# Kernel optimization log

Measured on AMD Instinct MI355X. Metric: run time of the kernel, lower is better.

## Reference

```python
import jax, jax.numpy as jnp
import numpy as np

BATCH, TIME, IN, HID = 32, 512, 512, 1024
THRESHOLD = 1.0
BETA = 1.0 / 2.0  # 1/tau


def setup_inputs() -> dict:
    key = jax.random.key(0)
    kx, kw, kb = jax.random.split(key, 3)
    x = jax.random.normal(kx, (BATCH, TIME, IN), dtype=jnp.float32)
    bound = 1.0 / np.sqrt(IN)  # nn.Linear default init range
    W = jax.random.uniform(kw, (HID, IN), minval=-bound, maxval=bound, dtype=jnp.float32)
    b = jax.random.uniform(kb, (HID,), minval=-bound, maxval=bound, dtype=jnp.float32)
    return {"x": x, "W": W, "b": b}


def reference(x, W, b):
    # Precompute all per-step linear projections in one big GEMM: [B,T,H]
    hidden = jnp.einsum("bti,hi->bth", x, W) + b

    def step(mem, h_t):
        # h_t: [B,H]
        mem = BETA * mem + h_t
        spk = (mem > THRESHOLD).astype(h_t.dtype)
        mem = mem * (1.0 - spk)  # hard reset
        return mem, spk

    mem0 = jnp.zeros((x.shape[0], W.shape[0]), dtype=x.dtype)
    # scan over time: [T,B,H]
    _, spikes = jax.lax.scan(step, mem0, jnp.swapaxes(hidden, 0, 1))
    return jnp.swapaxes(spikes, 0, 1)  # [B,T,H]
```

## Files before the change

kernel.cpp:

```cpp
#include <hip/hip_runtime.h>

#define BATCH 32
#define TIME  512
#define INF   512
#define HIDF  1024

#define MBT  128
#define NBH  128
#define KCH  16
#define NCH  (INF / KCH)
#define TILEF (MBT * KCH)

#define GLD16(g, l) __builtin_amdgcn_global_load_lds(                      \
    (const __attribute__((address_space(1))) void*)(g),                    \
    (__attribute__((address_space(3))) void*)(l), 16, 0, 0)

__global__ __launch_bounds__(256, 2)
void snn_gemm_seqfma(const float* __restrict__ x, const float* __restrict__ W,
                     const float* __restrict__ bias, float* __restrict__ hidden) {
    __shared__ __align__(16) float xs[2 * TILEF];
    __shared__ __align__(16) float ws[2 * TILEF];

    const int tid = threadIdx.x;
    const int l   = tid & 63;
    const int wv  = __builtin_amdgcn_readfirstlane(tid >> 6);
    const int lx  = l & 7;
    const int ly  = (l >> 3) & 7;
    const int bt0 = blockIdx.y * MBT;
    const int h0  = blockIdx.x * NBH;
    const int wbt = 64 * (wv >> 1);
    const int wh  = 64 * (wv & 1);

    const int rl = l >> 2;
    const int qs = l & 3;
    const int g0 = ((rl & 1) << 3) | (rl >> 1);
    const int wA = 2 * wv;
    const int wB = 2 * wv + 1;
    const int rA = wA * 16 + g0;
    const int rB = wB * 16 + g0;
    const int qA = qs ^ (wA & 3);
    const int qB = qs ^ (wB & 3);
    const float* xgA = x + (size_t)(bt0 + rA) * INF + qA * 4;
    const float* xgB = x + (size_t)(bt0 + rB) * INF + qB * 4;
    const float* wgA = W + (size_t)(h0 + rA) * INF + qA * 4;
    const float* wgB = W + (size_t)(h0 + rB) * INF + qB * 4;
    const int dOffA = (32 * wv) * KCH;
    const int dOffB = dOffA + 16 * KCH;

    GLD16(xgA, xs + dOffA);
    GLD16(xgB, xs + dOffB);
    GLD16(wgA, ws + dOffA);
    GLD16(wgB, ws + dOffB);

    float acc[8][8];
    #pragma unroll
    for (int r = 0; r < 8; ++r)
        #pragma unroll
        for (int c = 0; c < 8; ++c) acc[r][c] = 0.0f;

    __syncthreads();

    const int xrow0 = wbt + (ly >> 1) * 16 + (ly & 1);
    const int wrow0 = wh  + (lx >> 1) * 16 + (lx & 1);
    const int xq = (ly >> 1) & 3;
    const int wq = (lx >> 1) & 3;

    for (int kc = 0; kc < NCH; ++kc) {
        const int p  = kc & 1;
        const int np = p ^ 1;

        if (kc + 1 < NCH) {
            const int so = (kc + 1) * KCH;
            float* xd = xs + np * TILEF;
            float* wd = ws + np * TILEF;
            GLD16(xgA + so, xd + dOffA);
            GLD16(xgB + so, xd + dOffB);
            GLD16(wgA + so, wd + dOffA);
            GLD16(wgB + so, wd + dOffB);
        }

        const float* xb = xs + p * TILEF;
        const float* wb = ws + p * TILEF;
        #pragma unroll
        for (int g = 0; g < 4; ++g) {
            const int gx_ = (g ^ xq) * 4;
            const int gw_ = (g ^ wq) * 4;
            const float* xr = xb + xrow0 * KCH + gx_;
            const float* wr = wb + wrow0 * KCH + gw_;
            float4 xf[8], wf[8];
            #pragma unroll
            for (int r = 0; r < 8; ++r)
                xf[r] = *(const float4*)(xr + r * 2 * KCH);
            #pragma unroll
            for (int c = 0; c < 8; ++c)
                wf[c] = *(const float4*)(wr + c * 2 * KCH);
            #pragma unroll
            for (int r = 0; r < 8; ++r)
                #pragma unroll
                for (int c = 0; c < 8; ++c)
                    acc[r][c] = __fmaf_rn(xf[r].x, wf[c].x, acc[r][c]);
            #pragma unroll
            for (int r = 0; r < 8; ++r)
                #pragma unroll
                for (int c = 0; c < 8; ++c)
                    acc[r][c] = __fmaf_rn(xf[r].y, wf[c].y, acc[r][c]);
            #pragma unroll
            for (int r = 0; r < 8; ++r)
                #pragma unroll
                for (int c = 0; c < 8; ++c)
                    acc[r][c] = __fmaf_rn(xf[r].z, wf[c].z, acc[r][c]);
            #pragma unroll
            for (int r = 0; r < 8; ++r)
                #pragma unroll
                for (int c = 0; c < 8; ++c)
                    acc[r][c] = __fmaf_rn(xf[r].w, wf[c].w, acc[r][c]);
        }
        __syncthreads();
    }

    float bv[8];
    #pragma unroll
    for (int c = 0; c < 8; ++c) bv[c] = bias[h0 + wh + lx * 8 + c];
    #pragma unroll
    for (int r = 0; r < 8; ++r) {
        float* orow = hidden + (size_t)(bt0 + wbt + ly * 8 + r) * HIDF
                             + h0 + wh + lx * 8;
        float4 o0, o1;
        o0.x = __fadd_rn(acc[r][0], bv[0]);
        o0.y = __fadd_rn(acc[r][1], bv[1]);
        o0.z = __fadd_rn(acc[r][2], bv[2]);
        o0.w = __fadd_rn(acc[r][3], bv[3]);
        o1.x = __fadd_rn(acc[r][4], bv[4]);
        o1.y = __fadd_rn(acc[r][5], bv[5]);
        o1.z = __fadd_rn(acc[r][6], bv[6]);
        o1.w = __fadd_rn(acc[r][7], bv[7]);
        ((float4*)orow)[0] = o0;
        ((float4*)orow)[1] = o1;
    }
}

#define SEG 32

__global__ __launch_bounds__(64)
void snn_scan_np(float* __restrict__ io) {
    const int n = blockIdx.x * 64 + threadIdx.x;
    const int b = n >> 10;
    const int h = n & 1023;
    float* p = io + (size_t)b * TIME * HIDF + h;

    float A[SEG], B[SEG];
    float mem = 0.0f;

    #pragma unroll
    for (int u = 0; u < SEG; ++u) A[u] = p[u * HIDF];

    for (int tb = 0; tb < TIME / SEG; tb += 2) {
        #pragma unroll
        for (int u = 0; u < SEG; ++u) B[u] = p[((tb + 1) * SEG + u) * HIDF];
        #pragma unroll
        for (int u = 0; u < SEG; ++u) {
            mem = __fadd_rn(__fmul_rn(0.5f, mem), A[u]);
            const bool s = mem > 1.0f;
            p[(tb * SEG + u) * HIDF] = s ? 1.0f : 0.0f;
            if (s) mem = 0.0f;
        }
        if (tb + 2 < TIME / SEG) {
            #pragma unroll
            for (int u = 0; u < SEG; ++u) A[u] = p[((tb + 2) * SEG + u) * HIDF];
        }
        #pragma unroll
        for (int u = 0; u < SEG; ++u) {
            mem = __fadd_rn(__fmul_rn(0.5f, mem), B[u]);
            const bool s = mem > 1.0f;
            p[((tb + 1) * SEG + u) * HIDF] = s ? 1.0f : 0.0f;
            if (s) mem = 0.0f;
        }
    }
}

extern "C" void kernel_launch(void* const* d_in, const int* in_sizes, int n_in,
                              void* d_out, int out_size, void* d_ws, size_t ws_size,
                              hipStream_t stream) {
    const float* x    = (const float*)d_in[0];
    const float* W    = (const float*)d_in[1];
    const float* bias = (const float*)d_in[2];
    float* out = (float*)d_out;

    dim3 g1(HIDF / NBH, (BATCH * TIME) / MBT);
    snn_gemm_seqfma<<<g1, 256, 0, stream>>>(x, W, bias, out);

    snn_scan_np<<<(BATCH * HIDF) / 64, 64, 0, stream>>>(out);
}
```

Measured before the change: 314.4 us.

## Give each wave private LDS tiles and replace block barriers with vmcnt waits

Each wave now stages its own 64-row slices of x and W into a private double-buffered LDS region. The per-chunk __syncthreads is replaced by a per-wave s_waitcnt vmcnt plus a scheduling barrier, and the last chunk is peeled out of the loop. The aim is to remove block-wide barrier stalls and let waves run independently. In exchange, LDS use per block doubles to 64KB, and x/W rows shared by waves in the same block are now fetched redundantly, which raises global and L2 load traffic.

```diff
diff --git a/kernel.cpp b/kernel.cpp
--- a/kernel.cpp
+++ b/kernel.cpp
@@ -9,17 +9,57 @@
 #define NBH  128
 #define KCH  16
 #define NCH  (INF / KCH)
-#define TILEF (MBT * KCH)
 
 #define GLD16(g, l) __builtin_amdgcn_global_load_lds(                      \
     (const __attribute__((address_space(1))) void*)(g),                    \
     (__attribute__((address_space(3))) void*)(l), 16, 0, 0)
 
+
+__device__ __forceinline__ void compute_chunk(const float* __restrict__ xb,
+                                              const float* __restrict__ wb,
+                                              int xrow0, int wrow0,
+                                              int xq, int wq,
+                                              float acc[8][8]) {
+    #pragma unroll
+    for (int g = 0; g < 4; ++g) {
+        const int gx_ = (g ^ xq) * 4;
+        const int gw_ = (g ^ wq) * 4;
+        const float* xr = xb + xrow0 * KCH + gx_;
+        const float* wr = wb + wrow0 * KCH + gw_;
+        float4 xf[8], wf[8];
+        #pragma unroll
+        for (int r = 0; r < 8; ++r)
+            xf[r] = *(const float4*)(xr + r * 2 * KCH);
+        #pragma unroll
+        for (int c = 0; c < 8; ++c)
+            wf[c] = *(const float4*)(wr + c * 2 * KCH);
+        #pragma unroll
+        for (int r = 0; r < 8; ++r)
+            #pragma unroll
+            for (int c = 0; c < 8; ++c)
+                acc[r][c] = __fmaf_rn(xf[r].x, wf[c].x, acc[r][c]);
+        #pragma unroll
+        for (int r = 0; r < 8; ++r)
+            #pragma unroll
+            for (int c = 0; c < 8; ++c)
+                acc[r][c] = __fmaf_rn(xf[r].y, wf[c].y, acc[r][c]);
+        #pragma unroll
+        for (int r = 0; r < 8; ++r)
+            #pragma unroll
+            for (int c = 0; c < 8; ++c)
+                acc[r][c] = __fmaf_rn(xf[r].z, wf[c].z, acc[r][c]);
+        #pragma unroll
+        for (int r = 0; r < 8; ++r)
+            #pragma unroll
+            for (int c = 0; c < 8; ++c)
+                acc[r][c] = __fmaf_rn(xf[r].w, wf[c].w, acc[r][c]);
+    }
+}
+
 __global__ __launch_bounds__(256, 2)
 void snn_gemm_seqfma(const float* __restrict__ x, const float* __restrict__ W,
                      const float* __restrict__ bias, float* __restrict__ hidden) {
-    __shared__ __align__(16) float xs[2 * TILEF];
-    __shared__ __align__(16) float ws[2 * TILEF];
+    __shared__ __align__(16) float lds[2][4][2][1024];
 
     const int tid = threadIdx.x;
     const int l   = tid & 63;
@@ -34,23 +74,23 @@
     const int rl = l >> 2;
     const int qs = l & 3;
     const int g0 = ((rl & 1) << 3) | (rl >> 1);
-    const int wA = 2 * wv;
-    const int wB = 2 * wv + 1;
-    const int rA = wA * 16 + g0;
-    const int rB = wB * 16 + g0;
-    const int qA = qs ^ (wA & 3);
-    const int qB = qs ^ (wB & 3);
-    const float* xgA = x + (size_t)(bt0 + rA) * INF + qA * 4;
-    const float* xgB = x + (size_t)(bt0 + rB) * INF + qB * 4;
-    const float* wgA = W + (size_t)(h0 + rA) * INF + qA * 4;
-    const float* wgB = W + (size_t)(h0 + rB) * INF + qB * 4;
-    const int dOffA = (32 * wv) * KCH;
-    const int dOffB = dOffA + 16 * KCH;
-
-    GLD16(xgA, xs + dOffA);
-    GLD16(xgB, xs + dOffB);
-    GLD16(wgA, ws + dOffA);
-    GLD16(wgB, ws + dOffB);
+    const float* px0 = x + (size_t)(bt0 + wbt +  0 + g0) * INF + ((qs ^ 0) * 4);
+    const float* px1 = x + (size_t)(bt0 + wbt + 16 + g0) * INF + ((qs ^ 1) * 4);
+    const float* px2 = x + (size_t)(bt0 + wbt + 32 + g0) * INF + ((qs ^ 2) * 4);
+    const float* px3 = x + (size_t)(bt0 + wbt + 48 + g0) * INF + ((qs ^ 3) * 4);
+    const float* pw0 = W + (size_t)(h0 + wh +  0 + g0) * INF + ((qs ^ 0) * 4);
+    const float* pw1 = W + (size_t)(h0 + wh + 16 + g0) * INF + ((qs ^ 1) * 4);
+    const float* pw2 = W + (size_t)(h0 + wh + 32 + g0) * INF + ((qs ^ 2) * 4);
+    const float* pw3 = W + (size_t)(h0 + wh + 48 + g0) * INF + ((qs ^ 3) * 4);
+
+    GLD16(px0, &lds[0][wv][0][0 * 256]);
+    GLD16(px1, &lds[0][wv][0][1 * 256]);
+    GLD16(px2, &lds[0][wv][0][2 * 256]);
+    GLD16(px3, &lds[0][wv][0][3 * 256]);
+    GLD16(pw0, &lds[0][wv][1][0 * 256]);
+    GLD16(pw1, &lds[0][wv][1][1 * 256]);
+    GLD16(pw2, &lds[0][wv][1][2 * 256]);
+    GLD16(pw3, &lds[0][wv][1][3 * 256]);
 
     float acc[8][8];
     #pragma unroll
@@ -58,65 +98,36 @@
         #pragma unroll
         for (int c = 0; c < 8; ++c) acc[r][c] = 0.0f;
 
-    __syncthreads();
-
-    const int xrow0 = wbt + (ly >> 1) * 16 + (ly & 1);
-    const int wrow0 = wh  + (lx >> 1) * 16 + (lx & 1);
+    const int xrow0 = (ly >> 1) * 16 + (ly & 1);
+    const int wrow0 = (lx >> 1) * 16 + (lx & 1);
     const int xq = (ly >> 1) & 3;
     const int wq = (lx >> 1) & 3;
 
-    for (int kc = 0; kc < NCH; ++kc) {
+    for (int kc = 0; kc < NCH - 1; ++kc) {
         const int p  = kc & 1;
         const int np = p ^ 1;
-
-        if (kc + 1 < NCH) {
-            const int so = (kc + 1) * KCH;
-            float* xd = xs + np * TILEF;
-            float* wd = ws + np * TILEF;
-            GLD16(xgA + so, xd + dOffA);
-            GLD16(xgB + so, xd + dOffB);
-            GLD16(wgA + so, wd + dOffA);
-            GLD16(wgB + so, wd + dOffB);
-        }
-
-        const float* xb = xs + p * TILEF;
-        const float* wb = ws + p * TILEF;
-        #pragma unroll
-        for (int g = 0; g < 4; ++g) {
-            const int gx_ = (g ^ xq) * 4;
-            const int gw_ = (g ^ wq) * 4;
-            const float* xr = xb + xrow0 * KCH + gx_;
-            const float* wr = wb + wrow0 * KCH + gw_;
-            float4 xf[8], wf[8];
-            #pragma unroll
-            for (int r = 0; r < 8; ++r)
-                xf[r] = *(const float4*)(xr + r * 2 * KCH);
-            #pragma unroll
-            for (int c = 0; c < 8; ++c)
-                wf[c] = *(const float4*)(wr + c * 2 * KCH);
-            #pragma unroll
-            for (int r = 0; r < 8; ++r)
-                #pragma unroll
-                for (int c = 0; c < 8; ++c)
-                    acc[r][c] = __fmaf_rn(xf[r].x, wf[c].x, acc[r][c]);
-            #pragma unroll
-            for (int r = 0; r < 8; ++r)
-                #pragma unroll
-                for (int c = 0; c < 8; ++c)
-                    acc[r][c] = __fmaf_rn(xf[r].y, wf[c].y, acc[r][c]);
-            #pragma unroll
-            for (int r = 0; r < 8; ++r)
-                #pragma unroll
-                for (int c = 0; c < 8; ++c)
-                    acc[r][c] = __fmaf_rn(xf[r].z, wf[c].z, acc[r][c]);
-            #pragma unroll
-            for (int r = 0; r < 8; ++r)
-                #pragma unroll
-                for (int c = 0; c < 8; ++c)
-                    acc[r][c] = __fmaf_rn(xf[r].w, wf[c].w, acc[r][c]);
-        }
-        __syncthreads();
-    }
+        const int so = (kc + 1) * KCH;
+
+        GLD16(px0 + so, &lds[np][wv][0][0 * 256]);
+        GLD16(px1 + so, &lds[np][wv][0][1 * 256]);
+        GLD16(px2 + so, &lds[np][wv][0][2 * 256]);
+        GLD16(px3 + so, &lds[np][wv][0][3 * 256]);
+        GLD16(pw0 + so, &lds[np][wv][1][0 * 256]);
+        GLD16(pw1 + so, &lds[np][wv][1][1 * 256]);
+        GLD16(pw2 + so, &lds[np][wv][1][2 * 256]);
+        GLD16(pw3 + so, &lds[np][wv][1][3 * 256]);
+
+        asm volatile("s_waitcnt vmcnt(8)" ::: "memory");
+        __builtin_amdgcn_sched_barrier(0);
+
+        compute_chunk(&lds[p][wv][0][0], &lds[p][wv][1][0],
+                      xrow0, wrow0, xq, wq, acc);
+    }
+
+    asm volatile("s_waitcnt vmcnt(0)" ::: "memory");
+    __builtin_amdgcn_sched_barrier(0);
+    compute_chunk(&lds[(NCH - 1) & 1][wv][0][0], &lds[(NCH - 1) & 1][wv][1][0],
+                  xrow0, wrow0, xq, wq, acc);
 
     float bv[8];
     #pragma unroll
```

Measured after the change: 315.3 us. Within noise of the previous version (+0.3%).

## Load W fragments directly from global into registers, dropping W LDS staging

Applied to the files above, without the earlier changes.

The W tile is no longer staged through shared memory. Each thread now reads its own 8 W rows straight from global memory (through L1/L2) as float4 values, double-buffered in registers and interleaved with the FMA groups. This removes the LDS traffic and LDS footprint for W. In exchange it adds redundant global loads, since 8 ly-lanes read the same W rows, and raises register pressure under launch_bounds(256,2), which may cause spills or longer exposed load latency.

```diff
diff --git a/kernel.cpp b/kernel.cpp
--- a/kernel.cpp
+++ b/kernel.cpp
@@ -15,11 +15,42 @@
     (const __attribute__((address_space(1))) void*)(g),                    \
     (__attribute__((address_space(3))) void*)(l), 16, 0, 0)
 
+
+#define LDW(dst, koff)                                                     \
+    dst[0] = *(const float4*)(pw0 + (koff));                               \
+    dst[1] = *(const float4*)(pw0 + 512 + (koff));                         \
+    dst[2] = *(const float4*)(pw1 + (koff));                               \
+    dst[3] = *(const float4*)(pw1 + 512 + (koff));                         \
+    dst[4] = *(const float4*)(pw2 + (koff));                               \
+    dst[5] = *(const float4*)(pw2 + 512 + (koff));                         \
+    dst[6] = *(const float4*)(pw3 + (koff));                               \
+    dst[7] = *(const float4*)(pw3 + 512 + (koff));
+
+#define LDX(dst, g)                                                        \
+    {                                                                      \
+        const float* xr_ = xb + xrow0 * KCH + ((g) ^ xq) * 4;              \
+        _Pragma("unroll")                                                  \
+        for (int r_ = 0; r_ < 8; ++r_)                                     \
+            dst[r_] = *(const float4*)(xr_ + r_ * 2 * KCH);                \
+    }
+
+#define FMA_COMP(xf, wf, COMP)                                             \
+    _Pragma("unroll")                                                      \
+    for (int r_ = 0; r_ < 8; ++r_)                                         \
+        _Pragma("unroll")                                                  \
+        for (int c_ = 0; c_ < 8; ++c_)                                     \
+            acc[r_][c_] = __fmaf_rn(xf[r_].COMP, wf[c_].COMP, acc[r_][c_]);
+
+#define FMA_GROUP(xf, wf)                                                  \
+    FMA_COMP(xf, wf, x)                                                    \
+    FMA_COMP(xf, wf, y)                                                    \
+    FMA_COMP(xf, wf, z)                                                    \
+    FMA_COMP(xf, wf, w)
+
 __global__ __launch_bounds__(256, 2)
 void snn_gemm_seqfma(const float* __restrict__ x, const float* __restrict__ W,
                      const float* __restrict__ bias, float* __restrict__ hidden) {
     __shared__ __align__(16) float xs[2 * TILEF];
-    __shared__ __align__(16) float ws[2 * TILEF];
 
     const int tid = threadIdx.x;
     const int l   = tid & 63;
@@ -42,15 +73,16 @@
     const int qB = qs ^ (wB & 3);
     const float* xgA = x + (size_t)(bt0 + rA) * INF + qA * 4;
     const float* xgB = x + (size_t)(bt0 + rB) * INF + qB * 4;
-    const float* wgA = W + (size_t)(h0 + rA) * INF + qA * 4;
-    const float* wgB = W + (size_t)(h0 + rB) * INF + qB * 4;
     const int dOffA = (32 * wv) * KCH;
     const int dOffB = dOffA + 16 * KCH;
 
+    const float* pw0 = W + (size_t)(h0 + wh + lx * 8 + 0) * INF;
+    const float* pw1 = W + (size_t)(h0 + wh + lx * 8 + 2) * INF;
+    const float* pw2 = W + (size_t)(h0 + wh + lx * 8 + 4) * INF;
+    const float* pw3 = W + (size_t)(h0 + wh + lx * 8 + 6) * INF;
+
     GLD16(xgA, xs + dOffA);
     GLD16(xgB, xs + dOffB);
-    GLD16(wgA, ws + dOffA);
-    GLD16(wgB, ws + dOffB);
 
     float acc[8][8];
     #pragma unroll
@@ -61,60 +93,35 @@
     __syncthreads();
 
     const int xrow0 = wbt + (ly >> 1) * 16 + (ly & 1);
-    const int wrow0 = wh  + (lx >> 1) * 16 + (lx & 1);
     const int xq = (ly >> 1) & 3;
-    const int wq = (lx >> 1) & 3;
 
     for (int kc = 0; kc < NCH; ++kc) {
         const int p  = kc & 1;
         const int np = p ^ 1;
+        const int k0 = kc * KCH;
 
         if (kc + 1 < NCH) {
-            const int so = (kc + 1) * KCH;
+            const int so = k0 + KCH;
             float* xd = xs + np * TILEF;
-            float* wd = ws + np * TILEF;
             GLD16(xgA + so, xd + dOffA);
             GLD16(xgB + so, xd + dOffB);
-            GLD16(wgA + so, wd + dOffA);
-            GLD16(wgB + so, wd + dOffB);
         }
 
         const float* xb = xs + p * TILEF;
-        const float* wb = ws + p * TILEF;
-        #pragma unroll
-        for (int g = 0; g < 4; ++g) {
-            const int gx_ = (g ^ xq) * 4;
-            const int gw_ = (g ^ wq) * 4;
-            const float* xr = xb + xrow0 * KCH + gx_;
-            const float* wr = wb + wrow0 * KCH + gw_;
-            float4 xf[8], wf[8];
-            #pragma unroll
-            for (int r = 0; r < 8; ++r)
-                xf[r] = *(const float4*)(xr + r * 2 * KCH);
-            #pragma unroll
-            for (int c = 0; c < 8; ++c)
-                wf[c] = *(const float4*)(wr + c * 2 * KCH);
-            #pragma unroll
-            for (int r = 0; r < 8; ++r)
-                #pragma unroll
-                for (int c = 0; c < 8; ++c)
-                    acc[r][c] = __fmaf_rn(xf[r].x, wf[c].x, acc[r][c]);
-            #pragma unroll
-            for (int r = 0; r < 8; ++r)
-                #pragma unroll
-                for (int c = 0; c < 8; ++c)
-                    acc[r][c] = __fmaf_rn(xf[r].y, wf[c].y, acc[r][c]);
-            #pragma unroll
-            for (int r = 0; r < 8; ++r)
-                #pragma unroll
-                for (int c = 0; c < 8; ++c)
-                    acc[r][c] = __fmaf_rn(xf[r].z, wf[c].z, acc[r][c]);
-            #pragma unroll
-            for (int r = 0; r < 8; ++r)
-                #pragma unroll
-                for (int c = 0; c < 8; ++c)
-                    acc[r][c] = __fmaf_rn(xf[r].w, wf[c].w, acc[r][c]);
-        }
+        float4 xf[8], wfA[8], wfB[8];
+        LDW(wfA, k0 + 0 * 4)
+        LDX(xf, 0)
+        LDW(wfB, k0 + 1 * 4)
+        FMA_GROUP(xf, wfA)
+        LDX(xf, 1)
+        LDW(wfA, k0 + 2 * 4)
+        FMA_GROUP(xf, wfB)
+        LDX(xf, 2)
+        LDW(wfB, k0 + 3 * 4)
+        FMA_GROUP(xf, wfA)
+        LDX(xf, 3)
+        FMA_GROUP(xf, wfB)
+
         __syncthreads();
     }
 
```

Result: slower. 692.4 us (+120.3%).
